# Performance work log

Hardware: AMD Instinct MI355X
Metric: run time of the kernel (lower is better)

Reference implementation:

```python
import jax, jax.numpy as jnp
import numpy as np

NUM_EXPERTS = 8
TOP_K = 2


def setup_inputs() -> dict:
    key = jax.random.key(0)
    k1, k2, k3, k4 = jax.random.split(key, 4)
    B, T, H, F = 4, 2048, 1024, 4096
    x = jax.random.normal(k1, (B, T, H), dtype=jnp.float32)
    gate_w = jax.random.normal(k2, (H, NUM_EXPERTS), dtype=jnp.float32) * 0.02
    w1 = jax.random.normal(k3, (NUM_EXPERTS, H, F), dtype=jnp.float32) * 0.02
    w2 = jax.random.normal(k4, (NUM_EXPERTS, F, H), dtype=jnp.float32) * 0.02
    return {"x": x, "gate_w": gate_w, "w1": w1, "w2": w2}


def moe_forward(x, gate_w, w1, w2):
    # Router: logits (B,T,E), top-k indices/weights
    logits = jnp.einsum("bth,he->bte", x, gate_w)
    top_logits, indices = jax.lax.top_k(logits, TOP_K)          # (B,T,K)
    weights = jax.nn.softmax(top_logits, axis=-1)               # (B,T,K)
    # Combine weights per expert: (B,T,E); zero where token not routed to e.
    combine = jnp.sum(
        jax.nn.one_hot(indices, NUM_EXPERTS, dtype=x.dtype) * weights[..., None],
        axis=2,
    )
    # Dense equivalent of masked gather/FFN/scatter-add: loop over the small
    # fixed expert set, accumulate weighted expert outputs. Zero combine
    # weight for unrouted tokens reproduces the masked dispatch exactly.
    out = jnp.zeros_like(x)
    for e in range(NUM_EXPERTS):
        h = jax.nn.relu(jnp.einsum("bth,hf->btf", x, w1[e]))
        y = jnp.einsum("btf,fh->bth", h, w2[e])
        out = out + combine[..., e:e + 1] * y
    return out, logits


def reference(x, gate_w, w1, w2):
    return moe_forward(x, gate_w, w1, w2)
```

## Files before the change

### kernel.cpp

```cpp
#include <hip/hip_runtime.h>
#include <hip/hip_bf16.h>
#include <stdint.h>

#define NE 8
#define NTOK 8192
#define HD 1024
#define FD 4096
#define NSLOT (NTOK * 2)

typedef __attribute__((ext_vector_type(4))) float floatx4;
typedef __attribute__((ext_vector_type(8))) __bf16 bf16x8;
typedef __attribute__((ext_vector_type(8))) unsigned short ushortx8;

__device__ __forceinline__ unsigned short f2bf(float f) {
    union { float f; unsigned u; } v; v.f = f;
    unsigned r = v.u + 0x7FFFu + ((v.u >> 16) & 1u);
    return (unsigned short)(r >> 16);
}

__device__ __forceinline__ void gload_lds16(const unsigned short* g, unsigned short* l) {
    __builtin_amdgcn_global_load_lds(
        (const __attribute__((address_space(1))) void*)g,
        (__attribute__((address_space(3))) void*)l,
        16, 0, 0);
}

__global__ void transpose_cast_kernel(const float* __restrict__ w, unsigned short* __restrict__ wt,
                                      int rows, int cols) {
    __shared__ unsigned short tile[64][66];
    int e = blockIdx.z;
    int r0 = blockIdx.y * 64;
    int c0 = blockIdx.x * 64;
    const float* ws = w + (size_t)e * rows * cols;
    unsigned short* wd = wt + (size_t)e * rows * cols;
    int tid = threadIdx.x;
#pragma unroll
    for (int j = 0; j < 4; j++) {
        int idx = j * 256 + tid;
        int r = idx >> 4;
        int c4 = (idx & 15) * 4;
        float4 v = *(const float4*)(ws + (size_t)(r0 + r) * cols + c0 + c4);
        ushort2 lo, hi;
        lo.x = f2bf(v.x); lo.y = f2bf(v.y);
        hi.x = f2bf(v.z); hi.y = f2bf(v.w);
        *(ushort2*)&tile[r][c4]     = lo;
        *(ushort2*)&tile[r][c4 + 2] = hi;
    }
    __syncthreads();
#pragma unroll
    for (int j = 0; j < 2; j++) {
        int idx = j * 256 + tid;
        int c = idx >> 3;
        int r8 = (idx & 7) * 8;
        ushortx8 o;
#pragma unroll
        for (int k = 0; k < 8; k++) o[k] = tile[r8 + k][c];
        *(ushortx8*)(wd + (size_t)(c0 + c) * rows + r0 + r8) = o;
    }
}

__global__ void router_kernel(const float* __restrict__ x, const float* __restrict__ gw,
                              float* __restrict__ logits, int* __restrict__ eid,
                              float* __restrict__ wts, unsigned short* __restrict__ xb) {
    int lane = threadIdx.x & 63;
    int t = blockIdx.x * 4 + (threadIdx.x >> 6);
    const float* xr = x + (size_t)t * HD;
    unsigned short* xbr = xb + (size_t)t * HD;
    float a0=0,a1=0,a2=0,a3=0,a4=0,a5=0,a6=0,a7=0;
    for (int c = lane; c < HD; c += 64) {
        float xv = xr[c];
        xbr[c] = f2bf(xv);
        const float4* g = (const float4*)(gw + (size_t)c * NE);
        float4 g0 = g[0], g1 = g[1];
        a0 += xv * g0.x; a1 += xv * g0.y; a2 += xv * g0.z; a3 += xv * g0.w;
        a4 += xv * g1.x; a5 += xv * g1.y; a6 += xv * g1.z; a7 += xv * g1.w;
    }
#pragma unroll
    for (int off = 32; off > 0; off >>= 1) {
        a0 += __shfl_xor(a0, off); a1 += __shfl_xor(a1, off);
        a2 += __shfl_xor(a2, off); a3 += __shfl_xor(a3, off);
        a4 += __shfl_xor(a4, off); a5 += __shfl_xor(a5, off);
        a6 += __shfl_xor(a6, off); a7 += __shfl_xor(a7, off);
    }
    if (lane == 0) {
        float l[8] = {a0,a1,a2,a3,a4,a5,a6,a7};
        float4 s0 = make_float4(a0,a1,a2,a3);
        float4 s1 = make_float4(a4,a5,a6,a7);
        ((float4*)(logits + (size_t)t * NE))[0] = s0;
        ((float4*)(logits + (size_t)t * NE))[1] = s1;
        int e0 = 0; float v0 = l[0];
#pragma unroll
        for (int e = 1; e < 8; e++) if (l[e] > v0) { v0 = l[e]; e0 = e; }
        int e1 = -1; float v1 = -3.4e38f;
#pragma unroll
        for (int e = 0; e < 8; e++) if (e != e0 && l[e] > v1) { v1 = l[e]; e1 = e; }
        float ex = __expf(v1 - v0);
        float dn = 1.f + ex;
        wts[2*t]   = 1.f / dn;
        wts[2*t+1] = ex / dn;
        eid[2*t]   = e0;
        eid[2*t+1] = e1;
    }
}

__global__ void build_perm_kernel(const int* __restrict__ eid, int* __restrict__ perm,
                                  int* __restrict__ counts) {
    int e = blockIdx.x;
    int lane = threadIdx.x;
    int base = 0;
    int* permE = perm + e * NTOK;
    for (int i0 = 0; i0 < NSLOT; i0 += 64) {
        int s = i0 + lane;
        bool match = (eid[s] == e);
        unsigned long long mask = __ballot(match);
        int pre = __popcll(mask & ((1ULL << lane) - 1ULL));
        if (match) permE[base + pre] = s;
        base += __popcll(mask);
    }
    if (lane == 0) counts[e] = base;
}

template<int KTOT, int NTOT, bool G1>
__global__ __launch_bounds__(256, 2)
void moe_gemm(const unsigned short* __restrict__ A,
              const unsigned short* __restrict__ Bt,
              unsigned short* __restrict__ Hout,
              float* __restrict__ Out,
              const int* __restrict__ counts,
              const int* __restrict__ perm,
              const float* __restrict__ wts) {
    int e = blockIdx.y >> 6;
    int mtile = blockIdx.y & 63;
    int cnt = counts[e];
    if (mtile * 128 >= cnt) return;
    int n0 = blockIdx.x * 128;

    __shared__ unsigned short lds[2 * 128 * 64];
    __shared__ int slotLds[128];
    __shared__ float wLds[128];

    int tid = threadIdx.x;
    int lane = tid & 63;
    int wv = tid >> 6;
    const int* permE = perm + e * NTOK + mtile * 128;

    if (tid < 128) {
        int s = (mtile * 128 + tid < cnt) ? permE[tid] : -1;
        slotLds[tid] = s;
        if (!G1) wLds[tid] = (s >= 0) ? wts[s] : 0.f;
    }

    const unsigned short* aRow[4];
    const unsigned short* bRow[4];
#pragma unroll
    for (int it = 0; it < 4; it++) {
        int r = it * 32 + (tid >> 3);
        int s = (mtile * 128 + r < cnt) ? permE[r] : permE[0];
        size_t arow = G1 ? (size_t)(s >> 1) : (size_t)s;
        aRow[it] = A + arow * KTOT;
        bRow[it] = Bt + ((size_t)e * NTOT + n0 + r) * KTOT;
    }
    int koff = ((tid & 7) ^ ((tid >> 3) & 7)) * 8;
    unsigned short* ldsA = lds;
    unsigned short* ldsB = lds + 128 * 64;
    int wbase = (tid & 192) * 8;

    floatx4 acc[4][4];
    floatx4 zero = {0.f, 0.f, 0.f, 0.f};
#pragma unroll
    for (int i = 0; i < 4; i++)
#pragma unroll
        for (int j = 0; j < 4; j++) acc[i][j] = zero;

    int m = lane & 15, quad = lane >> 4;
    int rA = (wv >> 1) * 64 + m;
    int rB = (wv & 1) * 64 + m;
    int xs = m & 7;

    for (int k0 = 0; k0 < KTOT; k0 += 64) {
#pragma unroll
        for (int it = 0; it < 4; it++)
            gload_lds16(aRow[it] + k0 + koff, ldsA + it * 2048 + wbase);
#pragma unroll
        for (int it = 0; it < 4; it++)
            gload_lds16(bRow[it] + k0 + koff, ldsB + it * 2048 + wbase);
        __builtin_amdgcn_s_waitcnt(0);
        __syncthreads();
#pragma unroll
        for (int kk = 0; kk < 2; kk++) {
            bf16x8 af[4], bfr[4];
#pragma unroll
            for (int mi = 0; mi < 4; mi++)
                af[mi] = *(const bf16x8*)(ldsA + (((rA + mi * 16) * 8 + ((kk * 4 + quad) ^ xs)) * 8));
#pragma unroll
            for (int ni = 0; ni < 4; ni++)
                bfr[ni] = *(const bf16x8*)(ldsB + (((rB + ni * 16) * 8 + ((kk * 4 + quad) ^ xs)) * 8));
#pragma unroll
            for (int mi = 0; mi < 4; mi++)
#pragma unroll
                for (int ni = 0; ni < 4; ni++)
                    acc[mi][ni] = __builtin_amdgcn_mfma_f32_16x16x32_bf16(af[mi], bfr[ni], acc[mi][ni], 0, 0, 0);
        }
        __syncthreads();
    }

    int colb = (wv & 1) * 64 + m;
    int rb = (wv >> 1) * 64 + quad * 4;
#pragma unroll
    for (int mi = 0; mi < 4; mi++) {
#pragma unroll
        for (int reg = 0; reg < 4; reg++) {
            int rl = rb + mi * 16 + reg;
            int s = slotLds[rl];
            if (s < 0) continue;
            if (G1) {
                unsigned short* hr = Hout + (size_t)s * NTOT + n0 + colb;
#pragma unroll
                for (int ni = 0; ni < 4; ni++) {
                    float v = acc[mi][ni][reg];
                    hr[ni * 16] = f2bf(v > 0.f ? v : 0.f);
                }
            } else {
                float w = wLds[rl];
                float* orow = Out + (size_t)(s >> 1) * NTOT + n0 + colb;
#pragma unroll
                for (int ni = 0; ni < 4; ni++)
                    atomicAdd(&orow[ni * 16], w * acc[mi][ni][reg]);
            }
        }
    }
}

extern "C" void kernel_launch(void* const* d_in, const int* in_sizes, int n_in,
                              void* d_out, int out_size, void* d_ws, size_t ws_size,
                              hipStream_t stream) {
    (void)in_sizes; (void)n_in; (void)out_size;
    const float* x  = (const float*)d_in[0];
    const float* gw = (const float*)d_in[1];
    const float* w1 = (const float*)d_in[2];
    const float* w2 = (const float*)d_in[3];
    float* out = (float*)d_out;
    float* logits = out + (size_t)NTOK * HD;

    char* ws = (char*)d_ws;
    int*   counts = (int*)ws;
    int*   perm   = (int*)(ws + 256);
    float* wts    = (float*)(ws + 256 + 262144);
    int*   eid    = (int*)(ws + 256 + 262144 + 65536);
    unsigned short* xb    = (unsigned short*)(ws + 458752);
    unsigned short* wtbuf = xb + (size_t)NTOK * HD;
    unsigned short* h     = wtbuf + (size_t)NE * HD * FD;
    size_t needed = 458752 + (size_t)NTOK*HD*2 + (size_t)NE*HD*FD*2 + (size_t)NSLOT*FD*2;
    if (ws_size < needed) return;

    hipMemsetAsync(out, 0, (size_t)NTOK * HD * sizeof(float), stream);

    transpose_cast_kernel<<<dim3(FD / 64, HD / 64, NE), 256, 0, stream>>>(w1, wtbuf, HD, FD);
    router_kernel<<<NTOK / 4, 256, 0, stream>>>(x, gw, logits, eid, wts, xb);
    build_perm_kernel<<<NE, 64, 0, stream>>>(eid, perm, counts);
    moe_gemm<HD, FD, true><<<dim3(FD / 128, NE * 64), 256, 0, stream>>>(
        xb, wtbuf, h, nullptr, counts, perm, wts);
    transpose_cast_kernel<<<dim3(HD / 64, FD / 64, NE), 256, 0, stream>>>(w2, wtbuf, FD, HD);
    moe_gemm<FD, HD, false><<<dim3(HD / 128, NE * 64), 256, 0, stream>>>(
        h, wtbuf, nullptr, out, counts, perm, wts);
}
```

Before: 767.1 us.

## Double-buffer MoE GEMM LDS, swizzle block order, parallelize permutation build

The grouped GEMM now double-buffers its LDS tiles, issuing the next k-tile's global-to-LDS loads before computing the current one, with partial vmcnt waits and s_setprio around the MFMA block. Block indices are remapped so that each expert's tiles are grouped into 8x8 supertiles, which is meant to improve L2 reuse of A and B. The serial 8-block permutation build is split into a per-segment count kernel and a fill kernel spread over 128 blocks. The slot and weight LDS caches are dropped in favour of direct global reads in the epilogue. LDS use doubles, which may reduce occupancy, and the hand-placed waits and barriers need to be exactly right.

```diff
diff --git a/kernel.cpp b/kernel.cpp
--- a/kernel.cpp
+++ b/kernel.cpp
@@ -7,6 +7,8 @@
 #define HD 1024
 #define FD 4096
 #define NSLOT (NTOK * 2)
+#define NSEG 16
+#define SEGLEN (NSLOT / NSEG)
 
 typedef __attribute__((ext_vector_type(4))) float floatx4;
 typedef __attribute__((ext_vector_type(8))) __bf16 bf16x8;
@@ -103,21 +105,39 @@
     }
 }
 
-__global__ void build_perm_kernel(const int* __restrict__ eid, int* __restrict__ perm,
-                                  int* __restrict__ counts) {
-    int e = blockIdx.x;
+__global__ void count_seg_kernel(const int* __restrict__ eid, int* __restrict__ segcnt) {
+    int e = blockIdx.x >> 4;
+    int seg = blockIdx.x & 15;
+    int lane = threadIdx.x;
+    int base = seg * SEGLEN;
+    int cnt = 0;
+    for (int i0 = 0; i0 < SEGLEN; i0 += 64) {
+        bool mt = (eid[base + i0 + lane] == e);
+        cnt += __popcll(__ballot(mt));
+    }
+    if (lane == 0) segcnt[blockIdx.x] = cnt;
+}
+
+__global__ void fill_perm_kernel(const int* __restrict__ eid, const int* __restrict__ segcnt,
+                                 int* __restrict__ perm, int* __restrict__ counts) {
+    int e = blockIdx.x >> 4;
+    int seg = blockIdx.x & 15;
     int lane = threadIdx.x;
     int base = 0;
+#pragma unroll
+    for (int s2 = 0; s2 < NSEG; s2++)
+        if (s2 < seg) base += segcnt[(e << 4) + s2];
     int* permE = perm + e * NTOK;
-    for (int i0 = 0; i0 < NSLOT; i0 += 64) {
-        int s = i0 + lane;
-        bool match = (eid[s] == e);
-        unsigned long long mask = __ballot(match);
+    int g0 = seg * SEGLEN;
+    for (int i0 = 0; i0 < SEGLEN; i0 += 64) {
+        int s = g0 + i0 + lane;
+        bool mt = (eid[s] == e);
+        unsigned long long mask = __ballot(mt);
         int pre = __popcll(mask & ((1ULL << lane) - 1ULL));
-        if (match) permE[base + pre] = s;
+        if (mt) permE[base + pre] = s;
         base += __popcll(mask);
     }
-    if (lane == 0) counts[e] = base;
+    if (lane == 0 && seg == NSEG - 1) counts[e] = base;
 }
 
 template<int KTOT, int NTOT, bool G1>
@@ -129,26 +149,25 @@
               const int* __restrict__ counts,
               const int* __restrict__ perm,
               const float* __restrict__ wts) {
-    int e = blockIdx.y >> 6;
-    int mtile = blockIdx.y & 63;
+    constexpr int GX = NTOT / 128;
+    constexpr int SN = GX / 8;
+    int bid = blockIdx.y * GX + blockIdx.x;
+    int e = bid & 7;
+    int i = bid >> 3;
+    int st = i >> 6, pos = i & 63;
+    int mg = st / SN, ng = st % SN;
+    int mtile = mg * 8 + (pos >> 3);
+    int n0 = (ng * 8 + (pos & 7)) * 128;
+
     int cnt = counts[e];
     if (mtile * 128 >= cnt) return;
-    int n0 = blockIdx.x * 128;
-
-    __shared__ unsigned short lds[2 * 128 * 64];
-    __shared__ int slotLds[128];
-    __shared__ float wLds[128];
+
+    __shared__ unsigned short lds[2 * 16384];
 
     int tid = threadIdx.x;
     int lane = tid & 63;
     int wv = tid >> 6;
     const int* permE = perm + e * NTOK + mtile * 128;
-
-    if (tid < 128) {
-        int s = (mtile * 128 + tid < cnt) ? permE[tid] : -1;
-        slotLds[tid] = s;
-        if (!G1) wLds[tid] = (s >= 0) ? wts[s] : 0.f;
-    }
 
     const unsigned short* aRow[4];
     const unsigned short* bRow[4];
@@ -161,47 +180,71 @@
         bRow[it] = Bt + ((size_t)e * NTOT + n0 + r) * KTOT;
     }
     int koff = ((tid & 7) ^ ((tid >> 3) & 7)) * 8;
-    unsigned short* ldsA = lds;
-    unsigned short* ldsB = lds + 128 * 64;
     int wbase = (tid & 192) * 8;
 
     floatx4 acc[4][4];
     floatx4 zero = {0.f, 0.f, 0.f, 0.f};
 #pragma unroll
-    for (int i = 0; i < 4; i++)
-#pragma unroll
-        for (int j = 0; j < 4; j++) acc[i][j] = zero;
+    for (int a = 0; a < 4; a++)
+#pragma unroll
+        for (int b = 0; b < 4; b++) acc[a][b] = zero;
 
     int m = lane & 15, quad = lane >> 4;
     int rA = (wv >> 1) * 64 + m;
     int rB = (wv & 1) * 64 + m;
     int xs = m & 7;
 
-    for (int k0 = 0; k0 < KTOT; k0 += 64) {
+    constexpr int NK = KTOT / 64;
+
+    auto stage = [&](int buf, int k0) {
+        unsigned short* la = &lds[buf * 16384];
+        unsigned short* lb = la + 8192;
 #pragma unroll
         for (int it = 0; it < 4; it++)
-            gload_lds16(aRow[it] + k0 + koff, ldsA + it * 2048 + wbase);
+            gload_lds16(aRow[it] + k0 + koff, la + it * 2048 + wbase);
 #pragma unroll
         for (int it = 0; it < 4; it++)
-            gload_lds16(bRow[it] + k0 + koff, ldsB + it * 2048 + wbase);
-        __builtin_amdgcn_s_waitcnt(0);
-        __syncthreads();
+            gload_lds16(bRow[it] + k0 + koff, lb + it * 2048 + wbase);
+    };
+
+    stage(0, 0);
+    int cur = 0;
+#pragma unroll 2
+    for (int kt = 0; kt < NK; kt++) {
+        if (kt + 1 < NK) {
+            stage(cur ^ 1, (kt + 1) * 64);
+            asm volatile("s_waitcnt vmcnt(8)" ::: "memory");
+        } else {
+            asm volatile("s_waitcnt vmcnt(0)" ::: "memory");
+        }
+        __builtin_amdgcn_sched_barrier(0);
+        __builtin_amdgcn_s_barrier();
+        __builtin_amdgcn_sched_barrier(0);
+
+        const unsigned short* la = &lds[cur * 16384];
+        const unsigned short* lb = la + 8192;
 #pragma unroll
         for (int kk = 0; kk < 2; kk++) {
             bf16x8 af[4], bfr[4];
 #pragma unroll
             for (int mi = 0; mi < 4; mi++)
-                af[mi] = *(const bf16x8*)(ldsA + (((rA + mi * 16) * 8 + ((kk * 4 + quad) ^ xs)) * 8));
+                af[mi] = *(const bf16x8*)(la + (((rA + mi * 16) * 8 + ((kk * 4 + quad) ^ xs)) * 8));
 #pragma unroll
             for (int ni = 0; ni < 4; ni++)
-                bfr[ni] = *(const bf16x8*)(ldsB + (((rB + ni * 16) * 8 + ((kk * 4 + quad) ^ xs)) * 8));
+                bfr[ni] = *(const bf16x8*)(lb + (((rB + ni * 16) * 8 + ((kk * 4 + quad) ^ xs)) * 8));
+            __builtin_amdgcn_s_setprio(1);
 #pragma unroll
             for (int mi = 0; mi < 4; mi++)
 #pragma unroll
                 for (int ni = 0; ni < 4; ni++)
                     acc[mi][ni] = __builtin_amdgcn_mfma_f32_16x16x32_bf16(af[mi], bfr[ni], acc[mi][ni], 0, 0, 0);
+            __builtin_amdgcn_s_setprio(0);
         }
-        __syncthreads();
+        asm volatile("s_waitcnt lgkmcnt(0)" ::: "memory");
+        __builtin_amdgcn_sched_barrier(0);
+        __builtin_amdgcn_s_barrier();
+        __builtin_amdgcn_sched_barrier(0);
+        cur ^= 1;
     }
 
     int colb = (wv & 1) * 64 + m;
@@ -211,8 +254,8 @@
 #pragma unroll
         for (int reg = 0; reg < 4; reg++) {
             int rl = rb + mi * 16 + reg;
-            int s = slotLds[rl];
-            if (s < 0) continue;
+            if (mtile * 128 + rl >= cnt) continue;
+            int s = permE[rl];
             if (G1) {
                 unsigned short* hr = Hout + (size_t)s * NTOT + n0 + colb;
 #pragma unroll
@@ -221,7 +264,7 @@
                     hr[ni * 16] = f2bf(v > 0.f ? v : 0.f);
                 }
             } else {
-                float w = wLds[rl];
+                float w = wts[s];
                 float* orow = Out + (size_t)(s >> 1) * NTOT + n0 + colb;
 #pragma unroll
                 for (int ni = 0; ni < 4; ni++)
@@ -247,6 +290,7 @@
     int*   perm   = (int*)(ws + 256);
     float* wts    = (float*)(ws + 256 + 262144);
     int*   eid    = (int*)(ws + 256 + 262144 + 65536);
+    int*   segcnt = (int*)(ws + 393472);
     unsigned short* xb    = (unsigned short*)(ws + 458752);
     unsigned short* wtbuf = xb + (size_t)NTOK * HD;
     unsigned short* h     = wtbuf + (size_t)NE * HD * FD;
@@ -257,7 +301,8 @@
 
     transpose_cast_kernel<<<dim3(FD / 64, HD / 64, NE), 256, 0, stream>>>(w1, wtbuf, HD, FD);
     router_kernel<<<NTOK / 4, 256, 0, stream>>>(x, gw, logits, eid, wts, xb);
-    build_perm_kernel<<<NE, 64, 0, stream>>>(eid, perm, counts);
+    count_seg_kernel<<<NE * NSEG, 64, 0, stream>>>(eid, segcnt);
+    fill_perm_kernel<<<NE * NSEG, 64, 0, stream>>>(eid, segcnt, perm, counts);
     moe_gemm<HD, FD, true><<<dim3(FD / 128, NE * 64), 256, 0, stream>>>(
         xb, wtbuf, h, nullptr, counts, perm, wts);
     transpose_cast_kernel<<<dim3(HD / 64, FD / 64, NE), 256, 0, stream>>>(w2, wtbuf, FD, HD);
```

Result: faster. 686.7 us (-10.5%).
